# Kernel optimization log

Hardware: AMD Instinct MI355X
Metric: run time of the kernel (lower is better)

## Reference

```python
import jax, jax.numpy as jnp
import numpy as np

B, N, Th, Td, Tw, Tp = 8, 3000, 24, 12, 24, 12
T2a, T2b, K = 64, 32, 3  # hidden temporal dims of the two STBlocks, Cheb order


def _laplacian(A):
    # PyG ChebConv with lambda_max=None -> lambda_max=2.0, sym normalization:
    # L_hat = 2L/lambda_max - I = -D^{-1/2} A D^{-1/2} with zero diagonal
    Aod = A * (1.0 - jnp.eye(A.shape[0], dtype=A.dtype))
    deg = Aod.sum(axis=1)
    dinv = jnp.where(deg > 0, deg ** -0.5, 0.0)
    return -(dinv[:, None] * Aod * dinv[None, :])


def _cheb(x, L, W, b):
    # Chebyshev graph conv, K=3. x: (B,N,Cin), L: (N,N), W: (K,Cin,Cout), b: (Cout,)
    Tx0 = x
    Tx1 = jnp.einsum('nm,bmi->bni', L, Tx0)
    Tx2 = 2.0 * jnp.einsum('nm,bmi->bni', L, Tx1) - Tx0
    out = (jnp.einsum('bni,io->bno', Tx0, W[0])
           + jnp.einsum('bni,io->bno', Tx1, W[1])
           + jnp.einsum('bni,io->bno', Tx2, W[2]))
    return out + b


def _tconv(x, w, b):
    # Conv1d(1, 1, 3, padding=1) over last axis. x: (B,N,T), w: (3,), b: scalar
    xp = jnp.pad(x, ((0, 0), (0, 0), (1, 1)))
    return w[0] * xp[..., :-2] + w[1] * xp[..., 1:-1] + w[2] * xp[..., 2:] + b


def _stblock(x, L, W, bg, cw, cb):
    x = jax.nn.relu(_cheb(x, L, W, bg))
    return jax.nn.relu(_tconv(x, cw, cb))


def _branch(X, L, W1, b1, c1w, c1b, W2, b2, c2w, c2b, WD, bD):
    x = X.reshape(X.shape[0], X.shape[1], X.shape[3])  # (B,N,T)
    x = _stblock(x, L, W1, b1, c1w, c1b)  # (B,N,64)
    x = _stblock(x, L, W2, b2, c2w, c2b)  # (B,N,32)
    return jax.nn.relu(x @ WD + bD)       # (B,N,Tp); forward only uses LinearD


def setup_inputs() -> dict:
    ks = jax.random.split(jax.random.key(0), 48)
    it = iter(range(48))

    def nrm(shape, s=1.0):
        return jax.random.normal(ks[next(it)], shape, jnp.float32) * s

    Xh = nrm((B, N, 1, Th))
    Xd = nrm((B, N, 1, Td))
    Xw = nrm((B, N, 1, Tw))
    u = jax.random.uniform(ks[next(it)], (N, N))
    w = jax.random.uniform(ks[next(it)], (N, N))
    A = jnp.where(u < 0.01, w, 0.0)
    A = 0.5 * (A + A.T)

    def gcn_p(ti, to):
        return nrm((K, ti, to), (2.0 / (ti + to)) ** 0.5), jnp.zeros((to,), jnp.float32)

    def conv_p():
        return nrm((K,), 0.4), nrm((), 0.1)

    Wh1, bh1 = gcn_p(Th, T2a); ch1w, ch1b = conv_p()
    Wh2, bh2 = gcn_p(T2a, T2b); ch2w, ch2b = conv_p()
    Wd1, bd1 = gcn_p(Td, T2a); cd1w, cd1b = conv_p()
    Wd2, bd2 = gcn_p(T2a, T2b); cd2w, cd2b = conv_p()
    Ww1, bw1 = gcn_p(Tw, T2a); cw1w, cw1b = conv_p()
    Ww2, bw2 = gcn_p(T2a, T2b); cw2w, cw2b = conv_p()
    WD = nrm((T2b, Tp), (2.0 / (T2b + Tp)) ** 0.5)
    bD = jnp.zeros((Tp,), jnp.float32)
    Fh = jax.random.uniform(ks[next(it)], (Tp,), jnp.float32)
    Fd = jax.random.uniform(ks[next(it)], (Tp,), jnp.float32)
    Fw = jax.random.uniform(ks[next(it)], (Tp,), jnp.float32)

    return dict(Xh=Xh, Xd=Xd, Xw=Xw, A=A,
                Wh1=Wh1, bh1=bh1, ch1w=ch1w, ch1b=ch1b, Wh2=Wh2, bh2=bh2, ch2w=ch2w, ch2b=ch2b,
                Wd1=Wd1, bd1=bd1, cd1w=cd1w, cd1b=cd1b, Wd2=Wd2, bd2=bd2, cd2w=cd2w, cd2b=cd2b,
                Ww1=Ww1, bw1=bw1, cw1w=cw1w, cw1b=cw1b, Ww2=Ww2, bw2=bw2, cw2w=cw2w, cw2b=cw2b,
                WD=WD, bD=bD, Fh=Fh, Fd=Fd, Fw=Fw)


def reference(Xh, Xd, Xw, A,
              Wh1, bh1, ch1w, ch1b, Wh2, bh2, ch2w, ch2b,
              Wd1, bd1, cd1w, cd1b, Wd2, bd2, cd2w, cd2b,
              Ww1, bw1, cw1w, cw1b, Ww2, bw2, cw2w, cw2b,
              WD, bD, Fh, Fd, Fw):
    L = _laplacian(A)
    Yh = _branch(Xh, L, Wh1, bh1, ch1w, ch1b, Wh2, bh2, ch2w, ch2b, WD, bD)
    Yd = _branch(Xd, L, Wd1, bd1, cd1w, cd1b, Wd2, bd2, cd2w, cd2b, WD, bD)
    Yw = _branch(Xw, L, Ww1, bw1, cw1w, cw1b, Ww2, bw2, cw2w, cw2b, WD, bD)
    Y = Fh * Yh + Fd * Yd + Fw * Yw  # Fusion: elementwise weighted sum over Tp
    return Y[:, :, None, :]  # (B,N,1,Tp)
```

## Files before the change

kernel.cpp:

```cpp
#include <hip/hip_runtime.h>

#define NN 3000
#define NB 8
#define TP 12
#define DMAX 128
#define F1T 480
#define F2T 768
#define Z1T 1536

struct BrW {
    const float *W1[3]; const float *b1[3]; const float *c1w[3]; const float *c1b[3];
    const float *W2[3]; const float *b2[3]; const float *c2w[3]; const float *c2b[3];
    const float *Fb[3];
};

__global__ void build_kernel(const float* __restrict__ A, int* __restrict__ colp,
                             float* __restrict__ valp, int* __restrict__ cnt,
                             float* __restrict__ dinv) {
    int n = blockIdx.x;
    int lane = threadIdx.x;
    const float* row = A + (size_t)n * NN;
    int base = 0;
    float s = 0.f;
    for (int start = 0; start < NN; start += 64) {
        int m = start + lane;
        float a = 0.f; bool nz = false;
        if (m < NN && m != n) {
            a = row[m];
            nz = (a != 0.f);
        }
        s += a;
        unsigned long long mask = __ballot(nz);
        int off = __popcll(mask & ((1ull << lane) - 1ull));
        if (nz) {
            int idx = base + off;
            if (idx < DMAX) { colp[n * DMAX + idx] = m; valp[n * DMAX + idx] = a; }
        }
        base += __popcll(mask);
    }
    for (int o = 32; o > 0; o >>= 1) s += __shfl_down(s, o);
    if (lane == 0) {
        cnt[n] = (base < DMAX) ? base : DMAX;
        dinv[n] = (s > 0.f) ? 1.0f / sqrtf(s) : 0.f;
    }
}

__global__ void scale_kernel(const int* __restrict__ colp, float* __restrict__ valp,
                             const int* __restrict__ cnt, const float* __restrict__ dinv) {
    int n = blockIdx.x;
    int j = threadIdx.x;
    if (j < cnt[n]) {
        int m = colp[n * DMAX + j];
        valp[n * DMAX + j] *= -dinv[n] * dinv[m];
    }
}

__global__ void pack_kernel(const float* __restrict__ Xh, const float* __restrict__ Xd,
                            const float* __restrict__ Xw, float* __restrict__ xcat) {
    int idx = blockIdx.x * blockDim.x + threadIdx.x;
    if (idx >= NN * F1T) return;
    int n = idx / F1T, r = idx % F1T;
    const float* src; int b, t, T;
    if (r < 192)      { src = Xh; T = 24; int rr = r;       b = rr / 24; t = rr % 24; }
    else if (r < 288) { src = Xd; T = 12; int rr = r - 192; b = rr / 12; t = rr % 12; }
    else              { src = Xw; T = 24; int rr = r - 288; b = rr / 24; t = rr % 24; }
    xcat[idx] = src[((size_t)b * NN + n) * T + t];
}

template <int F, int SLICE, int EPI>
__global__ void spmm_kernel(const int* __restrict__ colp, const float* __restrict__ valp,
                            const int* __restrict__ cnt, const float* __restrict__ x,
                            const float* __restrict__ aux, float* __restrict__ y) {
    int nwg = gridDim.x;
    int q = nwg >> 3;
    int bid = blockIdx.x;
    int w = (bid & 7) * q + (bid >> 3);
    int slice = w / NN;
    int n = w - slice * NN;
    int f = slice * SLICE + threadIdx.x;

    __shared__ int   scol[DMAX];
    __shared__ float sval[DMAX];
    int c = cnt[n];
    if (threadIdx.x < DMAX) {
        int j = threadIdx.x;
        bool ok = j < c;
        scol[j] = ok ? colp[n * DMAX + j] * F : 0;
        sval[j] = ok ? valp[n * DMAX + j] : 0.f;
    }
    __syncthreads();
    int c16 = (c + 15) & ~15;
    float a0 = 0.f, a1 = 0.f, a2 = 0.f, a3 = 0.f;
    float a4 = 0.f, a5 = 0.f, a6 = 0.f, a7 = 0.f;
    if (f < F) {
        for (int i = 0; i < c16; i += 16) {
            float g[16], w16[16];
            #pragma unroll
            for (int u = 0; u < 16; ++u) {
                int cc = scol[i + u];
                w16[u] = sval[i + u];
                g[u] = x[cc + f];
            }
            a0 += w16[0] * g[0];   a1 += w16[1] * g[1];
            a2 += w16[2] * g[2];   a3 += w16[3] * g[3];
            a4 += w16[4] * g[4];   a5 += w16[5] * g[5];
            a6 += w16[6] * g[6];   a7 += w16[7] * g[7];
            a0 += w16[8] * g[8];   a1 += w16[9] * g[9];
            a2 += w16[10] * g[10]; a3 += w16[11] * g[11];
            a4 += w16[12] * g[12]; a5 += w16[13] * g[13];
            a6 += w16[14] * g[14]; a7 += w16[15] * g[15];
        }
    }
    if (f >= F) return;
    float acc = ((a0 + a1) + (a2 + a3)) + ((a4 + a5) + (a6 + a7));
    size_t o = (size_t)n * F + f;
    if (EPI == 1) acc = 2.f * acc - aux[o];
    else if (EPI == 2) acc = aux[o] + 2.f * acc;
    y[o] = acc;
}

template <int T, int OFF, int BROFF>
__device__ __forceinline__ void combine1_gemm_body(
        int tile, const float* __restrict__ xcat, const float* __restrict__ t1cat,
        const float* __restrict__ t2cat, float* __restrict__ z1cat,
        const float* __restrict__ W, const float* __restrict__ bg,
        const float* __restrict__ cw, const float* __restrict__ cb,
        float* sW, float* sX) {
    constexpr int K = 3 * T;
    constexpr int LDA = K + 1;
    int tid = threadIdx.x;
    for (int i = tid; i < K * 64; i += 256) sW[i] = W[i];
    int n0 = tile * 12;
    #pragma unroll
    for (int s = 0; s < 3; ++s) {
        const float* src = (s == 0) ? xcat : (s == 1) ? t1cat : t2cat;
        for (int i = tid; i < 96 * T; i += 256) {
            int n_l = i / (8 * T), rem = i % (8 * T);
            int b = rem / T, ii = rem % T;
            float v = src[(size_t)(n0 + n_l) * F1T + OFF + b * T + ii];
            sX[(n_l * 8 + b) * LDA + s * T + ii] = v;
        }
    }
    __syncthreads();

    int rq = tid >> 3;
    int g  = tid & 7;
    float acc[3][8];
    #pragma unroll
    for (int r = 0; r < 3; ++r)
        #pragma unroll
        for (int j = 0; j < 8; ++j) acc[r][j] = 0.f;

    #pragma unroll 4
    for (int k = 0; k < K; ++k) {
        const float4* wr = reinterpret_cast<const float4*>(sW + k * 64 + g * 8);
        float4 wa = wr[0], wb = wr[1];
        #pragma unroll
        for (int r = 0; r < 3; ++r) {
            float zv = sX[(rq * 3 + r) * LDA + k];
            acc[r][0] += zv * wa.x; acc[r][1] += zv * wa.y;
            acc[r][2] += zv * wa.z; acc[r][3] += zv * wa.w;
            acc[r][4] += zv * wb.x; acc[r][5] += zv * wb.y;
            acc[r][6] += zv * wb.z; acc[r][7] += zv * wb.w;
        }
    }

    float bgv[8];
    #pragma unroll
    for (int j = 0; j < 8; ++j) bgv[j] = bg[g * 8 + j];
    float w0 = cw[0], w1 = cw[1], w2 = cw[2], bb = cb[0];

    #pragma unroll
    for (int r = 0; r < 3; ++r) {
        float z[8];
        #pragma unroll
        for (int j = 0; j < 8; ++j) z[j] = fmaxf(acc[r][j] + bgv[j], 0.f);
        float zl = __shfl_up(z[7], 1);
        float zr = __shfl_down(z[0], 1);
        float o[8];
        #pragma unroll
        for (int j = 0; j < 8; ++j) {
            float left  = (j > 0) ? z[j - 1] : ((g > 0) ? zl : 0.f);
            float right = (j < 7) ? z[j + 1] : ((g < 7) ? zr : 0.f);
            o[j] = fmaxf(w0 * left + w1 * z[j] + w2 * right + bb, 0.f);
        }
        int unit = tile * 96 + rq * 3 + r;
        int n = unit >> 3, b = unit & 7;
        float* dst = z1cat + (size_t)n * Z1T + BROFF + b * 64 + g * 8;
        reinterpret_cast<float4*>(dst)[0] = make_float4(o[0], o[1], o[2], o[3]);
        reinterpret_cast<float4*>(dst)[1] = make_float4(o[4], o[5], o[6], o[7]);
    }
}

__global__ void __launch_bounds__(256)
combine1_all_kernel(const float* __restrict__ xcat, const float* __restrict__ t1cat,
                    const float* __restrict__ t2cat, float* __restrict__ z1cat, BrW P) {
    __shared__ float sW[72 * 64];
    __shared__ float sX[96 * 73];
    int b = blockIdx.x;
    if (b < 250) {
        combine1_gemm_body<24, 0, 0>(b, xcat, t1cat, t2cat, z1cat,
                                     P.W1[0], P.b1[0], P.c1w[0], P.c1b[0], sW, sX);
    } else if (b < 500) {
        combine1_gemm_body<12, 192, 512>(b - 250, xcat, t1cat, t2cat, z1cat,
                                         P.W1[1], P.b1[1], P.c1w[1], P.c1b[1], sW, sX);
    } else {
        combine1_gemm_body<24, 288, 1024>(b - 500, xcat, t1cat, t2cat, z1cat,
                                          P.W1[2], P.b1[2], P.c1w[2], P.c1b[2], sW, sX);
    }
}

#define GR 96
__global__ void __launch_bounds__(256, 2)
gemmy_kernel(const float* __restrict__ z1cat, float* __restrict__ y1cat,
             float* __restrict__ y2cat, float* __restrict__ c0cat, BrW P) {
    int tile = blockIdx.x;
    int br = blockIdx.y;
    __shared__ float sW[64 * 96];
    __shared__ float sZ[GR][65];
    const float* W = P.W2[br];
    for (int i = threadIdx.x; i < 6144; i += 256) {
        int k = i / 96, c = i % 96;
        int j = c / 3, m = c % 3;
        sW[i] = W[m * 2048 + k * 32 + j];
    }
    int row0 = tile * GR;
    for (int i = threadIdx.x; i < GR * 64; i += 256) {
        int r = i >> 6, k = i & 63;
        int rg = row0 + r;
        int n = rg >> 3, b = rg & 7;
        sZ[r][k] = z1cat[(size_t)n * Z1T + br * 512 + b * 64 + k];
    }
    __syncthreads();

    int rq = threadIdx.x >> 3;
    int g = threadIdx.x & 7;
    float acc[3][12];
    #pragma unroll
    for (int rr = 0; rr < 3; ++rr)
        #pragma unroll
        for (int j = 0; j < 12; ++j) acc[rr][j] = 0.f;

    #pragma unroll 4
    for (int k = 0; k < 64; ++k) {
        const float4* wr = reinterpret_cast<const float4*>(sW + k * 96 + g * 12);
        float4 wa = wr[0], wb = wr[1], wc = wr[2];
        #pragma unroll
        for (int rr = 0; rr < 3; ++rr) {
            float zv = sZ[rq * 3 + rr][k];
            acc[rr][0] += zv * wa.x; acc[rr][1] += zv * wa.y;
            acc[rr][2] += zv * wa.z; acc[rr][3] += zv * wa.w;
            acc[rr][4] += zv * wb.x; acc[rr][5] += zv * wb.y;
            acc[rr][6] += zv * wb.z; acc[rr][7] += zv * wb.w;
            acc[rr][8] += zv * wc.x; acc[rr][9] += zv * wc.y;
            acc[rr][10] += zv * wc.z; acc[rr][11] += zv * wc.w;
        }
    }

    const float* b2 = P.b2[br];
    float bj0 = b2[g * 4 + 0], bj1 = b2[g * 4 + 1], bj2 = b2[g * 4 + 2], bj3 = b2[g * 4 + 3];
    #pragma unroll
    for (int rr = 0; rr < 3; ++rr) {
        int rg = row0 + rq * 3 + rr;
        int n = rg >> 3, b = rg & 7;
        size_t obase = (size_t)n * F2T + br * 256 + b * 32;
        float bj[4] = {bj0, bj1, bj2, bj3};
        #pragma unroll
        for (int jj = 0; jj < 4; ++jj) {
            int j = g * 4 + jj;
            float a0 = acc[rr][jj * 3 + 0], a1 = acc[rr][jj * 3 + 1], a2 = acc[rr][jj * 3 + 2];
            y1cat[obase + j] = a1;
            y2cat[obase + j] = a2;
            c0cat[obase + j] = a0 - a2 + bj[jj];
        }
    }
}

__global__ void combine2_final_kernel(const float* __restrict__ c0cat,
                                      const float* __restrict__ vcat,
                                      const float* __restrict__ WD, const float* __restrict__ bD,
                                      float* __restrict__ out, BrW P) {
    int n = blockIdx.x;
    __shared__ float z2[3][NB][32];
    int unit = threadIdx.x >> 5;
    int co = threadIdx.x & 31;
    int br = unit >> 3, b = unit & 7;
    size_t o = (size_t)n * F2T + br * 256 + b * 32 + co;
    float a = fmaxf(c0cat[o] + vcat[o], 0.f);
    float left  = __shfl_up(a, 1);
    float right = __shfl_down(a, 1);
    if (co == 0) left = 0.f;
    if (co == 31) right = 0.f;
    float w0 = P.c2w[br][0], w1 = P.c2w[br][1], w2 = P.c2w[br][2], bb = P.c2b[br][0];
    z2[br][b][co] = fmaxf(w0 * left + w1 * a + w2 * right + bb, 0.f);
    __syncthreads();
    if (threadIdx.x < NB * TP) {
        int b2 = threadIdx.x / TP, tp = threadIdx.x % TP;
        float y = 0.f;
        for (int brr = 0; brr < 3; ++brr) {
            float s = bD[tp];
            const float* zz = z2[brr][b2];
            for (int c = 0; c < 32; ++c) s += zz[c] * WD[c * TP + tp];
            y += fmaxf(s, 0.f) * P.Fb[brr][tp];
        }
        out[((size_t)b2 * NN + n) * TP + tp] = y;
    }
}


static inline size_t align256(size_t x) { return (x + 255) & ~(size_t)255; }

extern "C" void kernel_launch(void* const* d_in, const int* in_sizes, int n_in,
                              void* d_out, int out_size, void* d_ws, size_t ws_size,
                              hipStream_t stream) {
    const float* Xh = (const float*)d_in[0];
    const float* Xd = (const float*)d_in[1];
    const float* Xw = (const float*)d_in[2];
    const float* A  = (const float*)d_in[3];
    const float* WD = (const float*)d_in[28];
    const float* bD = (const float*)d_in[29];

    BrW P;
    for (int br = 0; br < 3; ++br) {
        int base = 4 + br * 8;
        P.W1[br]  = (const float*)d_in[base + 0];
        P.b1[br]  = (const float*)d_in[base + 1];
        P.c1w[br] = (const float*)d_in[base + 2];
        P.c1b[br] = (const float*)d_in[base + 3];
        P.W2[br]  = (const float*)d_in[base + 4];
        P.b2[br]  = (const float*)d_in[base + 5];
        P.c2w[br] = (const float*)d_in[base + 6];
        P.c2b[br] = (const float*)d_in[base + 7];
        P.Fb[br]  = (const float*)d_in[30 + br];
    }

    char* p = (char*)d_ws;
    int*   colp  = (int*)p;   p += align256((size_t)NN * DMAX * 4);
    float* valp  = (float*)p; p += align256((size_t)NN * DMAX * 4);
    int*   cnt   = (int*)p;   p += align256(NN * 4);
    float* dinv  = (float*)p; p += align256(NN * 4);
    float* xcat  = (float*)p; p += align256((size_t)NN * F1T * 4);
    float* t1cat = (float*)p; p += align256((size_t)NN * F1T * 4);
    float* t2cat = (float*)p; p += align256((size_t)NN * F1T * 4);
    float* z1cat = (float*)p; p += align256((size_t)NN * Z1T * 4);
    float* y1cat = (float*)p; p += align256((size_t)NN * F2T * 4);
    float* y2cat = (float*)p; p += align256((size_t)NN * F2T * 4);
    float* c0cat = (float*)p; p += align256((size_t)NN * F2T * 4);
    float* scat  = (float*)p; p += align256((size_t)NN * F2T * 4);
    float* vcat  = (float*)p; p += align256((size_t)NN * F2T * 4);

    build_kernel<<<NN, 64, 0, stream>>>(A, colp, valp, cnt, dinv);
    scale_kernel<<<NN, DMAX, 0, stream>>>(colp, valp, cnt, dinv);
    pack_kernel<<<(NN * F1T + 255) / 256, 256, 0, stream>>>(Xh, Xd, Xw, xcat);

    spmm_kernel<F1T, 256, 0><<<6000, 256, 0, stream>>>(colp, valp, cnt, xcat, nullptr, t1cat);
    spmm_kernel<F1T, 256, 1><<<6000, 256, 0, stream>>>(colp, valp, cnt, t1cat, xcat, t2cat);
    combine1_all_kernel<<<750, 256, 0, stream>>>(xcat, t1cat, t2cat, z1cat, P);

    gemmy_kernel<<<dim3(250, 3), 256, 0, stream>>>(z1cat, y1cat, y2cat, c0cat, P);
    spmm_kernel<F2T, 128, 2><<<18000, 128, 0, stream>>>(colp, valp, cnt, y2cat, y1cat, scat);
    spmm_kernel<F2T, 128, 0><<<18000, 128, 0, stream>>>(colp, valp, cnt, scat, nullptr, vcat);

    combine2_final_kernel<<<NN, 768, 0, stream>>>(c0cat, vcat, WD, bD, (float*)d_out, P);
}
```

Before: 174.7 us.

## Fuse first-block combine with second-block GEMM and widen SpMM gather unroll

Merges the first ST-block combine (Cheb GEMM, ReLU, temporal conv) with the second block's weight GEMM in one kernel. The intermediate z1 tile now stays in shared memory instead of going through a global buffer, which removes one launch and a write and read of z1cat. The SpMM inner loop is also unrolled to 32 neighbours per step to expose more gather loads in flight. The costs are extra register pressure and a larger padded tail when a row has few neighbours. The fused kernel also reuses one shared buffer across both phases, which adds a barrier.

```diff
diff --git a/kernel.cpp b/kernel.cpp
--- a/kernel.cpp
+++ b/kernel.cpp
@@ -89,26 +89,25 @@
         sval[j] = ok ? valp[n * DMAX + j] : 0.f;
     }
     __syncthreads();
-    int c16 = (c + 15) & ~15;
+    int c32 = (c + 31) & ~31;
     float a0 = 0.f, a1 = 0.f, a2 = 0.f, a3 = 0.f;
     float a4 = 0.f, a5 = 0.f, a6 = 0.f, a7 = 0.f;
     if (f < F) {
-        for (int i = 0; i < c16; i += 16) {
-            float g[16], w16[16];
+        for (int i = 0; i < c32; i += 32) {
+            float g[32], w32[32];
             #pragma unroll
-            for (int u = 0; u < 16; ++u) {
+            for (int u = 0; u < 32; ++u) {
                 int cc = scol[i + u];
-                w16[u] = sval[i + u];
+                w32[u] = sval[i + u];
                 g[u] = x[cc + f];
             }
-            a0 += w16[0] * g[0];   a1 += w16[1] * g[1];
-            a2 += w16[2] * g[2];   a3 += w16[3] * g[3];
-            a4 += w16[4] * g[4];   a5 += w16[5] * g[5];
-            a6 += w16[6] * g[6];   a7 += w16[7] * g[7];
-            a0 += w16[8] * g[8];   a1 += w16[9] * g[9];
-            a2 += w16[10] * g[10]; a3 += w16[11] * g[11];
-            a4 += w16[12] * g[12]; a5 += w16[13] * g[13];
-            a6 += w16[14] * g[14]; a7 += w16[15] * g[15];
+            #pragma unroll
+            for (int u = 0; u < 32; u += 8) {
+                a0 += w32[u + 0] * g[u + 0]; a1 += w32[u + 1] * g[u + 1];
+                a2 += w32[u + 2] * g[u + 2]; a3 += w32[u + 3] * g[u + 3];
+                a4 += w32[u + 4] * g[u + 4]; a5 += w32[u + 5] * g[u + 5];
+                a6 += w32[u + 6] * g[u + 6]; a7 += w32[u + 7] * g[u + 7];
+            }
         }
     }
     if (f >= F) return;
@@ -119,17 +118,19 @@
     y[o] = acc;
 }
 
-template <int T, int OFF, int BROFF>
-__device__ __forceinline__ void combine1_gemm_body(
-        int tile, const float* __restrict__ xcat, const float* __restrict__ t1cat,
-        const float* __restrict__ t2cat, float* __restrict__ z1cat,
-        const float* __restrict__ W, const float* __restrict__ bg,
-        const float* __restrict__ cw, const float* __restrict__ cb,
-        float* sW, float* sX) {
+#define SZ_LDA 68
+template <int T, int OFF>
+__device__ __forceinline__ void fused1_body(
+        int tile, int br, const float* __restrict__ xcat, const float* __restrict__ t1cat,
+        const float* __restrict__ t2cat, float* __restrict__ y1cat,
+        float* __restrict__ y2cat, float* __restrict__ c0cat, const BrW& P, float* smem) {
     constexpr int K = 3 * T;
     constexpr int LDA = K + 1;
     int tid = threadIdx.x;
-    for (int i = tid; i < K * 64; i += 256) sW[i] = W[i];
+    float* sW1 = smem;
+    float* sX  = smem + K * 64;
+    const float* W1 = P.W1[br];
+    for (int i = tid; i < K * 64; i += 256) sW1[i] = W1[i];
     int n0 = tile * 12;
     #pragma unroll
     for (int s = 0; s < 3; ++s) {
@@ -137,8 +138,8 @@
         for (int i = tid; i < 96 * T; i += 256) {
             int n_l = i / (8 * T), rem = i % (8 * T);
             int b = rem / T, ii = rem % T;
-            float v = src[(size_t)(n0 + n_l) * F1T + OFF + b * T + ii];
-            sX[(n_l * 8 + b) * LDA + s * T + ii] = v;
+            sX[(n_l * 8 + b) * LDA + s * T + ii] =
+                src[(size_t)(n0 + n_l) * F1T + OFF + b * T + ii];
         }
     }
     __syncthreads();
@@ -153,7 +154,7 @@
 
     #pragma unroll 4
     for (int k = 0; k < K; ++k) {
-        const float4* wr = reinterpret_cast<const float4*>(sW + k * 64 + g * 8);
+        const float4* wr = reinterpret_cast<const float4*>(sW1 + k * 64 + g * 8);
         float4 wa = wr[0], wb = wr[1];
         #pragma unroll
         for (int r = 0; r < 3; ++r) {
@@ -167,9 +168,10 @@
 
     float bgv[8];
     #pragma unroll
-    for (int j = 0; j < 8; ++j) bgv[j] = bg[g * 8 + j];
-    float w0 = cw[0], w1 = cw[1], w2 = cw[2], bb = cb[0];
-
+    for (int j = 0; j < 8; ++j) bgv[j] = P.b1[br][g * 8 + j];
+    float w0 = P.c1w[br][0], w1 = P.c1w[br][1], w2 = P.c1w[br][2], bb = P.c1b[br][0];
+
+    float o[3][8];
     #pragma unroll
     for (int r = 0; r < 3; ++r) {
         float z[8];
@@ -177,103 +179,79 @@
         for (int j = 0; j < 8; ++j) z[j] = fmaxf(acc[r][j] + bgv[j], 0.f);
         float zl = __shfl_up(z[7], 1);
         float zr = __shfl_down(z[0], 1);
-        float o[8];
         #pragma unroll
         for (int j = 0; j < 8; ++j) {
             float left  = (j > 0) ? z[j - 1] : ((g > 0) ? zl : 0.f);
             float right = (j < 7) ? z[j + 1] : ((g < 7) ? zr : 0.f);
-            o[j] = fmaxf(w0 * left + w1 * z[j] + w2 * right + bb, 0.f);
-        }
+            o[r][j] = fmaxf(w0 * left + w1 * z[j] + w2 * right + bb, 0.f);
+        }
+    }
+    __syncthreads();
+
+    float* sZ  = smem;
+    float* sW2 = smem + 96 * SZ_LDA;
+    #pragma unroll
+    for (int r = 0; r < 3; ++r) {
+        float* dst = sZ + (rq * 3 + r) * SZ_LDA + g * 8;
+        reinterpret_cast<float4*>(dst)[0] = make_float4(o[r][0], o[r][1], o[r][2], o[r][3]);
+        reinterpret_cast<float4*>(dst)[1] = make_float4(o[r][4], o[r][5], o[r][6], o[r][7]);
+    }
+    const float* W2 = P.W2[br];
+    for (int i = tid; i < 6144; i += 256) {
+        int k = i / 96, cc = i % 96;
+        int j = cc / 3, m = cc % 3;
+        sW2[i] = W2[m * 2048 + k * 32 + j];
+    }
+    __syncthreads();
+
+    float acc2[3][12];
+    #pragma unroll
+    for (int r = 0; r < 3; ++r)
+        #pragma unroll
+        for (int j = 0; j < 12; ++j) acc2[r][j] = 0.f;
+
+    #pragma unroll 4
+    for (int k = 0; k < 64; ++k) {
+        const float4* wr = reinterpret_cast<const float4*>(sW2 + k * 96 + g * 12);
+        float4 wa = wr[0], wb = wr[1], wc = wr[2];
+        #pragma unroll
+        for (int r = 0; r < 3; ++r) {
+            float zv = sZ[(rq * 3 + r) * SZ_LDA + k];
+            acc2[r][0] += zv * wa.x;  acc2[r][1] += zv * wa.y;
+            acc2[r][2] += zv * wa.z;  acc2[r][3] += zv * wa.w;
+            acc2[r][4] += zv * wb.x;  acc2[r][5] += zv * wb.y;
+            acc2[r][6] += zv * wb.z;  acc2[r][7] += zv * wb.w;
+            acc2[r][8] += zv * wc.x;  acc2[r][9] += zv * wc.y;
+            acc2[r][10] += zv * wc.z; acc2[r][11] += zv * wc.w;
+        }
+    }
+
+    const float* b2 = P.b2[br];
+    #pragma unroll
+    for (int r = 0; r < 3; ++r) {
         int unit = tile * 96 + rq * 3 + r;
         int n = unit >> 3, b = unit & 7;
-        float* dst = z1cat + (size_t)n * Z1T + BROFF + b * 64 + g * 8;
-        reinterpret_cast<float4*>(dst)[0] = make_float4(o[0], o[1], o[2], o[3]);
-        reinterpret_cast<float4*>(dst)[1] = make_float4(o[4], o[5], o[6], o[7]);
-    }
-}
-
-__global__ void __launch_bounds__(256)
-combine1_all_kernel(const float* __restrict__ xcat, const float* __restrict__ t1cat,
-                    const float* __restrict__ t2cat, float* __restrict__ z1cat, BrW P) {
-    __shared__ float sW[72 * 64];
-    __shared__ float sX[96 * 73];
-    int b = blockIdx.x;
-    if (b < 250) {
-        combine1_gemm_body<24, 0, 0>(b, xcat, t1cat, t2cat, z1cat,
-                                     P.W1[0], P.b1[0], P.c1w[0], P.c1b[0], sW, sX);
-    } else if (b < 500) {
-        combine1_gemm_body<12, 192, 512>(b - 250, xcat, t1cat, t2cat, z1cat,
-                                         P.W1[1], P.b1[1], P.c1w[1], P.c1b[1], sW, sX);
-    } else {
-        combine1_gemm_body<24, 288, 1024>(b - 500, xcat, t1cat, t2cat, z1cat,
-                                          P.W1[2], P.b1[2], P.c1w[2], P.c1b[2], sW, sX);
-    }
-}
-
-#define GR 96
-__global__ void __launch_bounds__(256, 2)
-gemmy_kernel(const float* __restrict__ z1cat, float* __restrict__ y1cat,
-             float* __restrict__ y2cat, float* __restrict__ c0cat, BrW P) {
-    int tile = blockIdx.x;
-    int br = blockIdx.y;
-    __shared__ float sW[64 * 96];
-    __shared__ float sZ[GR][65];
-    const float* W = P.W2[br];
-    for (int i = threadIdx.x; i < 6144; i += 256) {
-        int k = i / 96, c = i % 96;
-        int j = c / 3, m = c % 3;
-        sW[i] = W[m * 2048 + k * 32 + j];
-    }
-    int row0 = tile * GR;
-    for (int i = threadIdx.x; i < GR * 64; i += 256) {
-        int r = i >> 6, k = i & 63;
-        int rg = row0 + r;
-        int n = rg >> 3, b = rg & 7;
-        sZ[r][k] = z1cat[(size_t)n * Z1T + br * 512 + b * 64 + k];
-    }
-    __syncthreads();
-
-    int rq = threadIdx.x >> 3;
-    int g = threadIdx.x & 7;
-    float acc[3][12];
-    #pragma unroll
-    for (int rr = 0; rr < 3; ++rr)
-        #pragma unroll
-        for (int j = 0; j < 12; ++j) acc[rr][j] = 0.f;
-
-    #pragma unroll 4
-    for (int k = 0; k < 64; ++k) {
-        const float4* wr = reinterpret_cast<const float4*>(sW + k * 96 + g * 12);
-        float4 wa = wr[0], wb = wr[1], wc = wr[2];
-        #pragma unroll
-        for (int rr = 0; rr < 3; ++rr) {
-            float zv = sZ[rq * 3 + rr][k];
-            acc[rr][0] += zv * wa.x; acc[rr][1] += zv * wa.y;
-            acc[rr][2] += zv * wa.z; acc[rr][3] += zv * wa.w;
-            acc[rr][4] += zv * wb.x; acc[rr][5] += zv * wb.y;
-            acc[rr][6] += zv * wb.z; acc[rr][7] += zv * wb.w;
-            acc[rr][8] += zv * wc.x; acc[rr][9] += zv * wc.y;
-            acc[rr][10] += zv * wc.z; acc[rr][11] += zv * wc.w;
-        }
-    }
-
-    const float* b2 = P.b2[br];
-    float bj0 = b2[g * 4 + 0], bj1 = b2[g * 4 + 1], bj2 = b2[g * 4 + 2], bj3 = b2[g * 4 + 3];
-    #pragma unroll
-    for (int rr = 0; rr < 3; ++rr) {
-        int rg = row0 + rq * 3 + rr;
-        int n = rg >> 3, b = rg & 7;
         size_t obase = (size_t)n * F2T + br * 256 + b * 32;
-        float bj[4] = {bj0, bj1, bj2, bj3};
         #pragma unroll
         for (int jj = 0; jj < 4; ++jj) {
             int j = g * 4 + jj;
-            float a0 = acc[rr][jj * 3 + 0], a1 = acc[rr][jj * 3 + 1], a2 = acc[rr][jj * 3 + 2];
+            float a0 = acc2[r][jj * 3 + 0], a1 = acc2[r][jj * 3 + 1], a2 = acc2[r][jj * 3 + 2];
             y1cat[obase + j] = a1;
             y2cat[obase + j] = a2;
-            c0cat[obase + j] = a0 - a2 + bj[jj];
-        }
-    }
+            c0cat[obase + j] = a0 - a2 + b2[j];
+        }
+    }
+}
+
+__global__ void __launch_bounds__(256)
+fused1_kernel(const float* __restrict__ xcat, const float* __restrict__ t1cat,
+              const float* __restrict__ t2cat, float* __restrict__ y1cat,
+              float* __restrict__ y2cat, float* __restrict__ c0cat, BrW P) {
+    __shared__ float smem[12672];
+    int b = blockIdx.x;
+    if (b < 250)      fused1_body<24, 0>(b, 0, xcat, t1cat, t2cat, y1cat, y2cat, c0cat, P, smem);
+    else if (b < 500) fused1_body<12, 192>(b - 250, 1, xcat, t1cat, t2cat, y1cat, y2cat, c0cat, P, smem);
+    else              fused1_body<24, 288>(b - 500, 2, xcat, t1cat, t2cat, y1cat, y2cat, c0cat, P, smem);
 }
 
 __global__ void combine2_final_kernel(const float* __restrict__ c0cat,
@@ -342,7 +320,6 @@
     float* xcat  = (float*)p; p += align256((size_t)NN * F1T * 4);
     float* t1cat = (float*)p; p += align256((size_t)NN * F1T * 4);
     float* t2cat = (float*)p; p += align256((size_t)NN * F1T * 4);
-    float* z1cat = (float*)p; p += align256((size_t)NN * Z1T * 4);
     float* y1cat = (float*)p; p += align256((size_t)NN * F2T * 4);
     float* y2cat = (float*)p; p += align256((size_t)NN * F2T * 4);
     float* c0cat = (float*)p; p += align256((size_t)NN * F2T * 4);
@@ -355,9 +332,9 @@
 
     spmm_kernel<F1T, 256, 0><<<6000, 256, 0, stream>>>(colp, valp, cnt, xcat, nullptr, t1cat);
     spmm_kernel<F1T, 256, 1><<<6000, 256, 0, stream>>>(colp, valp, cnt, t1cat, xcat, t2cat);
-    combine1_all_kernel<<<750, 256, 0, stream>>>(xcat, t1cat, t2cat, z1cat, P);
-
-    gemmy_kernel<<<dim3(250, 3), 256, 0, stream>>>(z1cat, y1cat, y2cat, c0cat, P);
+
+    fused1_kernel<<<750, 256, 0, stream>>>(xcat, t1cat, t2cat, y1cat, y2cat, c0cat, P);
+
     spmm_kernel<F2T, 128, 2><<<18000, 128, 0, stream>>>(colp, valp, cnt, y2cat, y1cat, scat);
     spmm_kernel<F2T, 128, 0><<<18000, 128, 0, stream>>>(colp, valp, cnt, scat, nullptr, vcat);
 
```

Result: no change. 175.4 us (+0.4%).
